# Optimization experiments

Measured on AMD Instinct MI355X. Metric: run time of the kernel, lower is better.

The kernel has to match this reference:

```python
import jax, jax.numpy as jnp
import numpy as np

MARGIN = 0.5  # init kwarg margin=0.5 (float -> fix_margin branch)

N, D, NUM_CLASSES = 8192, 128, 512


def setup_inputs() -> dict:
    key = jax.random.key(0)
    k1, k2 = jax.random.split(key)
    embeds = jax.random.normal(k1, (N, D), dtype=jnp.float32)
    labels = jax.random.randint(k2, (N,), 0, NUM_CLASSES)
    return {"embeds": embeds, "labels": labels}


def reference(embeds, labels):
    n = embeds.shape[0]
    # --- batch-hard mining (detached in original: .detach().cpu().numpy()) ---
    # Euclidean pairwise distances via Gram trick (avoids [N,N,D] intermediate).
    sq = jnp.sum(embeds * embeds, axis=1)  # [N]
    d2 = sq[:, None] + sq[None, :] - 2.0 * (embeds @ embeds.T)  # [N,N]
    dist = jnp.sqrt(jnp.maximum(d2, 0.0))
    dist = jax.lax.stop_gradient(dist)

    same = labels[:, None] == labels[None, :]  # [N,N]
    eye = jnp.eye(n, dtype=bool)
    pos_mask = same & ~eye          # same label, not self
    neg_mask = ~same                # different label (diag excluded since same there)

    pos_idx = jnp.argmax(jnp.where(pos_mask, dist, -jnp.inf), axis=1)  # hardest positive
    neg_idx = jnp.argmin(jnp.where(neg_mask, dist, jnp.inf), axis=1)   # hardest negative

    # --- margin loss with metric='sqeuclidean' (gradients flow through gathers) ---
    dp = embeds - embeds[pos_idx]
    dn = embeds - embeds[neg_idx]
    ap = jnp.sum(dp * dp, axis=1)
    an = jnp.sum(dn * dn, axis=1)
    return jnp.mean(jax.nn.relu(ap - an + MARGIN))
```

## Files before the change

### kernel.cpp

```cpp
#include <hip/hip_runtime.h>
#include <stdint.h>

#define NROWS 8192
#define DIM 128
#define NCHUNK 16
#define MARGIN 0.5f

typedef short short8 __attribute__((ext_vector_type(8)));
typedef float f32x4 __attribute__((ext_vector_type(4)));
typedef int   int4v __attribute__((ext_vector_type(4)));
typedef float f4v   __attribute__((ext_vector_type(4)));

static __device__ __forceinline__ unsigned short f2bf(float f) {
    union { float f; unsigned u; } x; x.f = f;
    unsigned u = x.u;
    return (unsigned short)((u + 0x7FFFu + ((u >> 16) & 1u)) >> 16);
}

__global__ __launch_bounds__(256) void prep(const float* __restrict__ emb,
                                            unsigned short* __restrict__ e16,
                                            float* __restrict__ cbuf,
                                            float* __restrict__ acc) {
    const int lane = threadIdx.x & 63;
    const int row = blockIdx.x * 4 + (threadIdx.x >> 6);
    const float2 v = reinterpret_cast<const float2*>(emb + row * DIM)[lane];
    float sq = v.x * v.x + v.y * v.y;
#pragma unroll
    for (int m = 1; m < 64; m <<= 1) sq += __shfl_xor(sq, m, 64);
    const unsigned pack = ((unsigned)f2bf(v.y) << 16) | (unsigned)f2bf(v.x);
    *reinterpret_cast<unsigned*>(e16 + row * DIM + lane * 2) = pack;
    if (lane == 0) cbuf[row] = sq + 512.0f;
    if (blockIdx.x == 0 && threadIdx.x == 0) *acc = 0.0f;
}

__global__ __launch_bounds__(256) void mine(const unsigned short* __restrict__ e16,
                                            const float* __restrict__ cbuf,
                                            const int* __restrict__ labels,
                                            unsigned* __restrict__ pos_part,
                                            unsigned* __restrict__ neg_part) {
    const int tid  = threadIdx.x;
    const int wave = tid >> 6;
    const int lane = tid & 63;
    const int l15  = lane & 15;
    const int lhi  = lane >> 4;
    const int iblk = blockIdx.x & 31;
    const int cblk = blockIdx.x >> 5;
    const int ibase = iblk * 256 + wave * 64;

    short8 bfrag[4][4];
    int labi[4];
#pragma unroll
    for (int it = 0; it < 4; ++it) {
        const int row = ibase + it * 16 + l15;
#pragma unroll
        for (int ks = 0; ks < 4; ++ks)
            bfrag[it][ks] = *reinterpret_cast<const short8*>(e16 + row * DIM + ks * 32 + lhi * 8);
        labi[it] = labels[row];
    }

    unsigned bp[4], bn[4];
#pragma unroll
    for (int it = 0; it < 4; ++it) { bp[it] = 8191u; bn[it] = 0x7F800000u; }

    const int jcbase = cblk * 512;
    for (int t = 0; t < 32; ++t) {
        const int jb = jcbase + t * 16;
        short8 af[4];
#pragma unroll
        for (int ks = 0; ks < 4; ++ks)
            af[ks] = *reinterpret_cast<const short8*>(e16 + (jb + l15) * DIM + ks * 32 + lhi * 8);
        const int4v labj = *reinterpret_cast<const int4v*>(labels + jb + lhi * 4);
        const f4v   c4   = *reinterpret_cast<const f4v*>(cbuf + jb + lhi * 4);

        f32x4 acc[4];
        const f32x4 z = {0.f, 0.f, 0.f, 0.f};
#pragma unroll
        for (int it = 0; it < 4; ++it)
            acc[it] = __builtin_amdgcn_mfma_f32_16x16x32_bf16(af[0], bfrag[it][0], z, 0, 0, 0);
#pragma unroll
        for (int ks = 1; ks < 4; ++ks)
#pragma unroll
            for (int it = 0; it < 4; ++it)
                acc[it] = __builtin_amdgcn_mfma_f32_16x16x32_bf16(af[ks], bfrag[it][ks], acc[it], 0, 0, 0);

        const int j0 = jb + lhi * 4;
        const unsigned pc0 = 8191u - (unsigned)j0;
        const unsigned nc0 = (unsigned)j0;
#pragma unroll
        for (int it = 0; it < 4; ++it) {
#pragma unroll
            for (int r = 0; r < 4; ++r) {
                const float g = fmaf(-2.0f, acc[it][r], c4[r]);
                union { float f; unsigned u; } cv; cv.f = g;
                const unsigned u = cv.u & 0xFFFFE000u;
                const unsigned pcand = u | (pc0 - (unsigned)r);
                const unsigned ncand = u | (nc0 + (unsigned)r);
                const bool eq = (labj[r] == labi[it]);
                const unsigned psel = eq ? pcand : 0u;
                const unsigned nsel = eq ? 0x7F800000u : ncand;
                bp[it] = bp[it] > psel ? bp[it] : psel;
                bn[it] = bn[it] < nsel ? bn[it] : nsel;
            }
        }
    }

#pragma unroll
    for (int it = 0; it < 4; ++it) {
        unsigned p = bp[it], n = bn[it];
        unsigned o;
        o = (unsigned)__shfl_xor((int)p, 16, 64); p = p > o ? p : o;
        o = (unsigned)__shfl_xor((int)p, 32, 64); p = p > o ? p : o;
        o = (unsigned)__shfl_xor((int)n, 16, 64); n = n < o ? n : o;
        o = (unsigned)__shfl_xor((int)n, 32, 64); n = n < o ? n : o;
        if (lane < 16) {
            pos_part[cblk * NROWS + ibase + it * 16 + lane] = p;
            neg_part[cblk * NROWS + ibase + it * 16 + lane] = n;
        }
    }
}

__global__ __launch_bounds__(256) void lossk(const float* __restrict__ emb,
                                             const unsigned* __restrict__ pos_part,
                                             const unsigned* __restrict__ neg_part,
                                             float* __restrict__ acc) {
    __shared__ float wsum[4];
    const int tid = threadIdx.x, lane = tid & 63, wave = tid >> 6;
    const int w = blockIdx.x * 4 + wave;
    float sum = 0.f;
    for (int itr = 0; itr < 8; ++itr) {
        const int i = itr * 1024 + w;
        unsigned p = pos_part[(lane & 15) * NROWS + i];
        unsigned n = neg_part[(lane & 15) * NROWS + i];
#pragma unroll
        for (int m = 1; m < 16; m <<= 1) {
            unsigned o;
            o = (unsigned)__shfl_xor((int)p, m, 64); p = p > o ? p : o;
            o = (unsigned)__shfl_xor((int)n, m, 64); n = n < o ? n : o;
        }
        const int jp = 8191 - (int)(p & 8191u);
        const int jn = (int)(n & 8191u);
        const float2 a = reinterpret_cast<const float2*>(emb + i  * DIM)[lane];
        const float2 b = reinterpret_cast<const float2*>(emb + jp * DIM)[lane];
        const float2 c = reinterpret_cast<const float2*>(emb + jn * DIM)[lane];
        float dx = a.x - b.x, dy = a.y - b.y;
        const float ap = dx * dx + dy * dy;
        dx = a.x - c.x; dy = a.y - c.y;
        const float an = dx * dx + dy * dy;
        float v = ap - an;
#pragma unroll
        for (int m = 1; m < 64; m <<= 1) v += __shfl_xor(v, m, 64);
        if (lane == 0) sum += fmaxf(v + MARGIN, 0.f);
    }
    if (lane == 0) wsum[wave] = sum;
    __syncthreads();
    if (tid == 0) atomicAdd(acc, wsum[0] + wsum[1] + wsum[2] + wsum[3]);
}

__global__ void fin(const float* __restrict__ acc, float* __restrict__ out) {
    out[0] = acc[0] * (1.0f / (float)NROWS);
}

extern "C" void kernel_launch(void* const* d_in, const int* in_sizes, int n_in,
                              void* d_out, int out_size, void* d_ws, size_t ws_size,
                              hipStream_t stream) {
    const float* emb   = (const float*)d_in[0];
    const int* labels  = (const int*)d_in[1];
    float* out = (float*)d_out;
    char* ws = (char*)d_ws;

    unsigned short* e16 = (unsigned short*)ws;
    float* cbuf         = (float*)(ws + 2097152);
    unsigned* pos_part  = (unsigned*)(ws + 2097152 + 32768);
    unsigned* neg_part  = pos_part + NCHUNK * NROWS;
    float* acc          = (float*)(neg_part + NCHUNK * NROWS);

    prep<<<2048, 256, 0, stream>>>(emb, e16, cbuf, acc);
    mine<<<512, 256, 0, stream>>>(e16, cbuf, labels, pos_part, neg_part);
    lossk<<<256, 256, 0, stream>>>(emb, pos_part, neg_part, acc);
    fin<<<1, 1, 0, stream>>>(acc, out);
}
```

Before: 110.5 us.

## Split mining into finer chunks, fold norm into MFMA init, drop atomic reduction

The mining grid grows from 512 to 4096 blocks: each wave now handles 32 rows against 128 columns, and 64 column chunks of partial results are written out. The per-column norm term is folded into the MFMA accumulator initial value (scaled by -0.5), so the packed sortable key comes straight from the accumulator. This removes the per-element FMA and the reversed-index encoding. The loss kernel now runs one row per wave and writes per-block sums that a 256-thread final kernel reduces, replacing the atomicAdd and its zero-initialisation. The trade-off is less reuse of B fragments per block and four times more partial-result traffic; tie-breaking between equal distances may also change.

After: 153.9 us. 39.3% more time.

```diff
diff --git a/kernel.cpp b/kernel.cpp
--- a/kernel.cpp
+++ b/kernel.cpp
@@ -3,13 +3,13 @@
 
 #define NROWS 8192
 #define DIM 128
-#define NCHUNK 16
+#define NCHUNK 64
+#define NIBLK 64
 #define MARGIN 0.5f
 
 typedef short short8 __attribute__((ext_vector_type(8)));
 typedef float f32x4 __attribute__((ext_vector_type(4)));
 typedef int   int4v __attribute__((ext_vector_type(4)));
-typedef float f4v   __attribute__((ext_vector_type(4)));
 
 static __device__ __forceinline__ unsigned short f2bf(float f) {
     union { float f; unsigned u; } x; x.f = f;
@@ -19,8 +19,7 @@
 
 __global__ __launch_bounds__(256) void prep(const float* __restrict__ emb,
                                             unsigned short* __restrict__ e16,
-                                            float* __restrict__ cbuf,
-                                            float* __restrict__ acc) {
+                                            float* __restrict__ cbuf) {
     const int lane = threadIdx.x & 63;
     const int row = blockIdx.x * 4 + (threadIdx.x >> 6);
     const float2 v = reinterpret_cast<const float2*>(emb + row * DIM)[lane];
@@ -30,7 +29,6 @@
     const unsigned pack = ((unsigned)f2bf(v.y) << 16) | (unsigned)f2bf(v.x);
     *reinterpret_cast<unsigned*>(e16 + row * DIM + lane * 2) = pack;
     if (lane == 0) cbuf[row] = sq + 512.0f;
-    if (blockIdx.x == 0 && threadIdx.x == 0) *acc = 0.0f;
 }
 
 __global__ __launch_bounds__(256) void mine(const unsigned short* __restrict__ e16,
@@ -43,14 +41,14 @@
     const int lane = tid & 63;
     const int l15  = lane & 15;
     const int lhi  = lane >> 4;
-    const int iblk = blockIdx.x & 31;
-    const int cblk = blockIdx.x >> 5;
-    const int ibase = iblk * 256 + wave * 64;
+    const int iblk = blockIdx.x & (NIBLK - 1);
+    const int cblk = blockIdx.x >> 6;
+    const int ibase = iblk * 128 + wave * 32;
 
-    short8 bfrag[4][4];
-    int labi[4];
+    short8 bfrag[2][4];
+    int labi[2];
 #pragma unroll
-    for (int it = 0; it < 4; ++it) {
+    for (int it = 0; it < 2; ++it) {
         const int row = ibase + it * 16 + l15;
 #pragma unroll
         for (int ks = 0; ks < 4; ++ks)
@@ -58,46 +56,41 @@
         labi[it] = labels[row];
     }
 
-    unsigned bp[4], bn[4];
-#pragma unroll
-    for (int it = 0; it < 4; ++it) { bp[it] = 8191u; bn[it] = 0x7F800000u; }
+    unsigned bp[2] = {0u, 0u};
+    unsigned bn[2] = {0xFFFFFFFFu, 0xFFFFFFFFu};
 
-    const int jcbase = cblk * 512;
-    for (int t = 0; t < 32; ++t) {
+    const int jcbase = cblk * 128;
+#pragma unroll 2
+    for (int t = 0; t < 8; ++t) {
         const int jb = jcbase + t * 16;
         short8 af[4];
 #pragma unroll
         for (int ks = 0; ks < 4; ++ks)
             af[ks] = *reinterpret_cast<const short8*>(e16 + (jb + l15) * DIM + ks * 32 + lhi * 8);
         const int4v labj = *reinterpret_cast<const int4v*>(labels + jb + lhi * 4);
-        const f4v   c4   = *reinterpret_cast<const f4v*>(cbuf + jb + lhi * 4);
+        const f32x4 c4   = *reinterpret_cast<const f32x4*>(cbuf + jb + lhi * 4);
+        const f32x4 cinit = c4 * -0.5f;
 
-        f32x4 acc[4];
-        const f32x4 z = {0.f, 0.f, 0.f, 0.f};
+        f32x4 acc[2];
 #pragma unroll
-        for (int it = 0; it < 4; ++it)
-            acc[it] = __builtin_amdgcn_mfma_f32_16x16x32_bf16(af[0], bfrag[it][0], z, 0, 0, 0);
+        for (int it = 0; it < 2; ++it)
+            acc[it] = __builtin_amdgcn_mfma_f32_16x16x32_bf16(af[0], bfrag[it][0], cinit, 0, 0, 0);
 #pragma unroll
         for (int ks = 1; ks < 4; ++ks)
 #pragma unroll
-            for (int it = 0; it < 4; ++it)
+            for (int it = 0; it < 2; ++it)
                 acc[it] = __builtin_amdgcn_mfma_f32_16x16x32_bf16(af[ks], bfrag[it][ks], acc[it], 0, 0, 0);
 
         const int j0 = jb + lhi * 4;
-        const unsigned pc0 = 8191u - (unsigned)j0;
-        const unsigned nc0 = (unsigned)j0;
 #pragma unroll
-        for (int it = 0; it < 4; ++it) {
+        for (int it = 0; it < 2; ++it) {
 #pragma unroll
             for (int r = 0; r < 4; ++r) {
-                const float g = fmaf(-2.0f, acc[it][r], c4[r]);
-                union { float f; unsigned u; } cv; cv.f = g;
-                const unsigned u = cv.u & 0xFFFFE000u;
-                const unsigned pcand = u | (pc0 - (unsigned)r);
-                const unsigned ncand = u | (nc0 + (unsigned)r);
+                union { float f; unsigned u; } cv; cv.f = acc[it][r];
+                const unsigned cand = (cv.u & 0xFFFFE000u) | ((unsigned)(j0 + r) & 0x1FFFu);
                 const bool eq = (labj[r] == labi[it]);
-                const unsigned psel = eq ? pcand : 0u;
-                const unsigned nsel = eq ? 0x7F800000u : ncand;
+                const unsigned psel = eq ? cand : 0u;
+                const unsigned nsel = eq ? 0xFFFFFFFFu : cand;
                 bp[it] = bp[it] > psel ? bp[it] : psel;
                 bn[it] = bn[it] < nsel ? bn[it] : nsel;
             }
@@ -105,7 +98,7 @@
     }
 
 #pragma unroll
-    for (int it = 0; it < 4; ++it) {
+    for (int it = 0; it < 2; ++it) {
         unsigned p = bp[it], n = bn[it];
         unsigned o;
         o = (unsigned)__shfl_xor((int)p, 16, 64); p = p > o ? p : o;
@@ -122,42 +115,47 @@
 __global__ __launch_bounds__(256) void lossk(const float* __restrict__ emb,
                                              const unsigned* __restrict__ pos_part,
                                              const unsigned* __restrict__ neg_part,
-                                             float* __restrict__ acc) {
+                                             float* __restrict__ bsum) {
     __shared__ float wsum[4];
     const int tid = threadIdx.x, lane = tid & 63, wave = tid >> 6;
-    const int w = blockIdx.x * 4 + wave;
-    float sum = 0.f;
-    for (int itr = 0; itr < 8; ++itr) {
-        const int i = itr * 1024 + w;
-        unsigned p = pos_part[(lane & 15) * NROWS + i];
-        unsigned n = neg_part[(lane & 15) * NROWS + i];
+    const int i = blockIdx.x * 4 + wave;
+    unsigned p = pos_part[lane * NROWS + i];
+    unsigned n = neg_part[lane * NROWS + i];
 #pragma unroll
-        for (int m = 1; m < 16; m <<= 1) {
-            unsigned o;
-            o = (unsigned)__shfl_xor((int)p, m, 64); p = p > o ? p : o;
-            o = (unsigned)__shfl_xor((int)n, m, 64); n = n < o ? n : o;
-        }
-        const int jp = 8191 - (int)(p & 8191u);
-        const int jn = (int)(n & 8191u);
-        const float2 a = reinterpret_cast<const float2*>(emb + i  * DIM)[lane];
-        const float2 b = reinterpret_cast<const float2*>(emb + jp * DIM)[lane];
-        const float2 c = reinterpret_cast<const float2*>(emb + jn * DIM)[lane];
-        float dx = a.x - b.x, dy = a.y - b.y;
-        const float ap = dx * dx + dy * dy;
-        dx = a.x - c.x; dy = a.y - c.y;
-        const float an = dx * dx + dy * dy;
-        float v = ap - an;
+    for (int m = 1; m < 64; m <<= 1) {
+        unsigned o;
+        o = (unsigned)__shfl_xor((int)p, m, 64); p = p > o ? p : o;
+        o = (unsigned)__shfl_xor((int)n, m, 64); n = n < o ? n : o;
+    }
+    const int jp = (int)(p & 8191u);
+    const int jn = (int)(n & 8191u);
+    const float2 a = reinterpret_cast<const float2*>(emb + i  * DIM)[lane];
+    const float2 b = reinterpret_cast<const float2*>(emb + jp * DIM)[lane];
+    const float2 c = reinterpret_cast<const float2*>(emb + jn * DIM)[lane];
+    float dx = a.x - b.x, dy = a.y - b.y;
+    const float ap = dx * dx + dy * dy;
+    dx = a.x - c.x; dy = a.y - c.y;
+    const float an = dx * dx + dy * dy;
+    float v = ap - an;
 #pragma unroll
-        for (int m = 1; m < 64; m <<= 1) v += __shfl_xor(v, m, 64);
-        if (lane == 0) sum += fmaxf(v + MARGIN, 0.f);
-    }
-    if (lane == 0) wsum[wave] = sum;
+    for (int m = 1; m < 64; m <<= 1) v += __shfl_xor(v, m, 64);
+    if (lane == 0) wsum[wave] = fmaxf(v + MARGIN, 0.f);
     __syncthreads();
-    if (tid == 0) atomicAdd(acc, wsum[0] + wsum[1] + wsum[2] + wsum[3]);
+    if (tid == 0) bsum[blockIdx.x] = wsum[0] + wsum[1] + wsum[2] + wsum[3];
 }
 
-__global__ void fin(const float* __restrict__ acc, float* __restrict__ out) {
-    out[0] = acc[0] * (1.0f / (float)NROWS);
+__global__ __launch_bounds__(256) void fin(const float* __restrict__ bsum,
+                                           float* __restrict__ out) {
+    __shared__ float wsum[4];
+    const int tid = threadIdx.x, lane = tid & 63, wave = tid >> 6;
+    float s = 0.f;
+#pragma unroll
+    for (int k = 0; k < 8; ++k) s += bsum[tid + k * 256];
+#pragma unroll
+    for (int m = 1; m < 64; m <<= 1) s += __shfl_xor(s, m, 64);
+    if (lane == 0) wsum[wave] = s;
+    __syncthreads();
+    if (tid == 0) out[0] = (wsum[0] + wsum[1] + wsum[2] + wsum[3]) * (1.0f / (float)NROWS);
 }
 
 extern "C" void kernel_launch(void* const* d_in, const int* in_sizes, int n_in,
@@ -169,13 +167,13 @@
     char* ws = (char*)d_ws;
 
     unsigned short* e16 = (unsigned short*)ws;
-    float* cbuf         = (float*)(ws + 2097152);
-    unsigned* pos_part  = (unsigned*)(ws + 2097152 + 32768);
-    unsigned* neg_part  = pos_part + NCHUNK * NROWS;
-    float* acc          = (float*)(neg_part + NCHUNK * NROWS);
+    float* cbuf         = (float*)(ws + (size_t)2097152);
+    unsigned* pos_part  = (unsigned*)(ws + (size_t)2097152 + 32768);
+    unsigned* neg_part  = pos_part + (size_t)NCHUNK * NROWS;
+    float* bsum         = (float*)(neg_part + (size_t)NCHUNK * NROWS);
 
-    prep<<<2048, 256, 0, stream>>>(emb, e16, cbuf, acc);
-    mine<<<512, 256, 0, stream>>>(e16, cbuf, labels, pos_part, neg_part);
-    lossk<<<256, 256, 0, stream>>>(emb, pos_part, neg_part, acc);
-    fin<<<1, 1, 0, stream>>>(acc, out);
+    prep<<<2048, 256, 0, stream>>>(emb, e16, cbuf);
+    mine<<<4096, 256, 0, stream>>>(e16, cbuf, labels, pos_part, neg_part);
+    lossk<<<2048, 256, 0, stream>>>(emb, pos_part, neg_part, bsum);
+    fin<<<1, 256, 0, stream>>>(bsum, out);
 }
```
